# Optimization experiments

Hardware: AMD Instinct MI355X
Metric: run time of the kernel (lower is better)

The kernel has to match this reference:

```python
import jax, jax.numpy as jnp
import numpy as np

L = 4            # n_layers
D_MODEL = 768
D_STATE = 16
D_CONV = 4
EXPAND = 2
D_INNER = EXPAND * D_MODEL      # 1536
DT_RANK = (D_MODEL + 15) // 16  # 48
B = 2
T = 2048
LN_EPS = 1e-5


def setup_inputs() -> dict:
    key = jax.random.key(0)
    ks = jax.random.split(key, 12)
    s = 0.02
    x = jax.random.normal(ks[0], (B, T, D_MODEL), dtype=jnp.float32)
    in_proj_w = jax.random.normal(ks[1], (L, 2 * D_INNER, D_MODEL), dtype=jnp.float32) * s
    conv_w = jax.random.normal(ks[2], (L, D_INNER, D_CONV), dtype=jnp.float32) * s
    conv_b = jnp.zeros((L, D_INNER), dtype=jnp.float32)
    x_proj_w = jax.random.normal(ks[3], (L, DT_RANK + 2 * D_STATE, D_INNER), dtype=jnp.float32) * s
    dt_proj_w = jax.random.normal(ks[4], (L, D_INNER, DT_RANK), dtype=jnp.float32) * s
    dt_proj_b = jax.random.normal(ks[5], (L, D_INNER), dtype=jnp.float32) * 0.1
    # Standard S4D-real init: A = -[1..d_state], stored as log
    A_log = jnp.log(jnp.broadcast_to(
        jnp.arange(1, D_STATE + 1, dtype=jnp.float32), (L, D_INNER, D_STATE)))
    D_param = jnp.ones((L, D_INNER), dtype=jnp.float32)
    out_proj_w = jax.random.normal(ks[6], (L, D_MODEL, D_INNER), dtype=jnp.float32) * s
    ln_g = jnp.ones((L, D_MODEL), dtype=jnp.float32)
    ln_b = jnp.zeros((L, D_MODEL), dtype=jnp.float32)
    return {"x": x, "in_proj_w": in_proj_w, "conv_w": conv_w, "conv_b": conv_b,
            "x_proj_w": x_proj_w, "dt_proj_w": dt_proj_w, "dt_proj_b": dt_proj_b,
            "A_log": A_log, "D_param": D_param, "out_proj_w": out_proj_w,
            "ln_g": ln_g, "ln_b": ln_b}


def _layernorm(x, g, b):
    mu = jnp.mean(x, axis=-1, keepdims=True)
    var = jnp.mean(jnp.square(x - mu), axis=-1, keepdims=True)
    return (x - mu) * jax.lax.rsqrt(var + LN_EPS) * g + b


def _mamba_layer(x, inw, convw, convb, xpw, dtw, dtb, A_log, Dp, outw):
    # x: [B,T,d_model]
    Tn = x.shape[1]
    xz = jnp.einsum('btd,ed->bte', x, inw)          # [B,T,2*d_inner]
    xin, z = jnp.split(xz, 2, axis=-1)              # each [B,T,d_inner]
    # causal depthwise conv1d over time (kernel d_conv)
    xp = jnp.pad(xin, ((0, 0), (D_CONV - 1, 0), (0, 0)))
    xc = convb
    for k in range(D_CONV):
        xc = xc + xp[:, k:k + Tn, :] * convw[:, k]
    xc = jax.nn.silu(xc)                            # [B,T,d_inner]
    dbl = jnp.einsum('bti,ei->bte', xc, xpw)        # [B,T,dt_rank+2*d_state]
    dt, Bs, Cs = jnp.split(dbl, [DT_RANK, DT_RANK + D_STATE], axis=-1)
    dt = jax.nn.softplus(jnp.einsum('btr,dr->btd', dt, dtw) + dtb)  # [B,T,d_inner]
    A = -jnp.exp(A_log)                             # [d_inner,d_state]
    dA = jnp.exp(jnp.einsum('btd,dn->btdn', dt, A))  # discretized A
    dBu = (dt * xc)[..., None] * Bs[:, :, None, :]   # [B,T,d_inner,d_state]

    def step(h, inp):
        dA_t, dBu_t, C_t = inp                      # [B,d,n],[B,d,n],[B,n]
        h = dA_t * h + dBu_t
        y = jnp.einsum('bdn,bn->bd', h, C_t)
        return h, y

    h0 = jnp.zeros((x.shape[0], D_INNER, D_STATE), x.dtype)
    _, ys = jax.lax.scan(step, h0,
                         (jnp.swapaxes(dA, 0, 1), jnp.swapaxes(dBu, 0, 1),
                          jnp.swapaxes(Cs, 0, 1)))
    y = jnp.swapaxes(ys, 0, 1) + xc * Dp            # skip connection D*u
    y = y * jax.nn.silu(z)                          # gate
    return jnp.einsum('bti,ei->bte', y, outw)       # [B,T,d_model]


def reference(x, in_proj_w, conv_w, conv_b, x_proj_w, dt_proj_w, dt_proj_b,
              A_log, D_param, out_proj_w, ln_g, ln_b):
    for l in range(L):
        residual = x
        h = _mamba_layer(x, in_proj_w[l], conv_w[l], conv_b[l], x_proj_w[l],
                         dt_proj_w[l], dt_proj_b[l], A_log[l], D_param[l],
                         out_proj_w[l])
        h = _layernorm(h, ln_g[l], ln_b[l])
        x = h + residual                            # dropout=0 -> identity
    return x
```

## Files before the change

### kernel.cpp

```cpp
#include <hip/hip_runtime.h>

#define T_LEN 2048
#define DM    768
#define DI    1536
#define DS    16
#define BB    2
#define NROWS (BB * T_LEN)
#define NCH   64
#define CLEN  32

#define OFF_DTB 0
#define OFF_A   6144
#define OFF_DP  104448
#define OFF_CW  110592
#define OFF_CB  135168
#define OFF_LG  141312
#define OFF_LB  144384
#define PRM_TOT 147456

typedef __attribute__((ext_vector_type(8))) short bh8;
typedef __attribute__((ext_vector_type(4))) float f32x4;

__device__ __forceinline__ float bf2f(unsigned short u) {
    return __uint_as_float(((unsigned)u) << 16);
}
__device__ __forceinline__ unsigned short f2bf(float f) {
    unsigned u = __float_as_uint(f);
    u += 0x7FFFu + ((u >> 16) & 1u);
    return (unsigned short)(u >> 16);
}
__device__ __forceinline__ float ldin(const void* p, long i, int bf) {
    return bf ? bf2f(((const unsigned short*)p)[i]) : ((const float*)p)[i];
}

__global__ void k_sniff(const unsigned short* __restrict__ x, int* __restrict__ flag) {
    __shared__ int cnt[4];
    int tid = threadIdx.x;
    int local = 0;
#pragma unroll
    for (int j = 0; j < 4; ++j) {
        unsigned short u = x[tid * 4 + j];
        int e = (u >> 7) & 0xFF;
        if (e >= 100 && e <= 140) local++;
    }
    for (int off = 32; off; off >>= 1) local += __shfl_down(local, off, 64);
    if ((tid & 63) == 0) cnt[tid >> 6] = local;
    __syncthreads();
    if (tid == 0) {
        int tot = cnt[0] + cnt[1] + cnt[2] + cnt[3];
        *flag = (tot >= 900) ? 1 : 0;
    }
}

__global__ void k_conv_bf16(unsigned short* __restrict__ dst, const void* __restrict__ src,
                            long n, const int* __restrict__ flag) {
    int bf = *flag;
    long i = (long)blockIdx.x * 256 + threadIdx.x;
    if (i < n) dst[i] = bf ? ((const unsigned short*)src)[i] : f2bf(((const float*)src)[i]);
}

__global__ void k_convx(unsigned short* __restrict__ xbf, float* __restrict__ xf,
                        const void* __restrict__ src, const int* __restrict__ flag) {
    int bf = *flag;
    long i = (long)blockIdx.x * 256 + threadIdx.x;
    if (i < (long)NROWS * DM) {
        float v = ldin(src, i, bf);
        xbf[i] = f2bf(v);
        xf[i]  = v;
    }
}

__global__ void k_conv_xpw(unsigned short* __restrict__ dst, const void* __restrict__ src,
                           const int* __restrict__ flag) {
    int bf = *flag;
    long i = (long)blockIdx.x * 256 + threadIdx.x;
    const long total = 4L * 128 * 1536;
    if (i < total) {
        int c = (int)(i % 1536);
        long rl = i / 1536;
        int r = (int)(rl % 128);
        int l = (int)(rl / 128);
        unsigned short v = 0;
        if (r < 80) {
            long si = ((long)l * 80 + r) * 1536 + c;
            v = bf ? ((const unsigned short*)src)[si] : f2bf(((const float*)src)[si]);
        }
        dst[i] = v;
    }
}

__global__ void k_conv_dtw(unsigned short* __restrict__ dst, const void* __restrict__ src,
                           const int* __restrict__ flag) {
    int bf = *flag;
    long i = (long)blockIdx.x * 256 + threadIdx.x;
    const long total = 4L * 1536 * 64;
    if (i < total) {
        int c = (int)(i % 64);
        long rl = i / 64;
        int d = (int)(rl % 1536);
        int l = (int)(rl / 1536);
        unsigned short v = 0;
        if (c < 48) {
            long si = ((long)l * 1536 + d) * 48 + c;
            v = bf ? ((const unsigned short*)src)[si] : f2bf(((const float*)src)[si]);
        }
        dst[i] = v;
    }
}

__global__ void k_params(float* __restrict__ prm, const void* dtb, const void* alog,
                         const void* dpar, const void* cw, const void* cb,
                         const void* lg, const void* lb, const int* __restrict__ flag) {
    int bf = *flag;
    int i = blockIdx.x * 256 + threadIdx.x;
    if (i >= PRM_TOT) return;
    float v;
    if (i < OFF_A)        v = ldin(dtb, i - OFF_DTB, bf);
    else if (i < OFF_DP)  v = -__expf(ldin(alog, i - OFF_A, bf));
    else if (i < OFF_CW)  v = ldin(dpar, i - OFF_DP, bf);
    else if (i < OFF_CB)  v = ldin(cw, i - OFF_CW, bf);
    else if (i < OFF_LG)  v = ldin(cb, i - OFF_CB, bf);
    else if (i < OFF_LB)  v = ldin(lg, i - OFF_LG, bf);
    else                  v = ldin(lb, i - OFF_LB, bf);
    prm[i] = v;
}

template <int EPI>
__global__ __launch_bounds__(256) void k_gemm128(const unsigned short* __restrict__ A,
                                                 const unsigned short* __restrict__ B,
                                                 float* __restrict__ C,
                                                 int M, int N, int K) {
    __shared__ __align__(16) unsigned short As[128 * 32];
    __shared__ __align__(16) unsigned short Bs[128 * 32];
    const int tid = threadIdx.x;
    const int lane = tid & 63, wid = tid >> 6;
    const int wm = wid >> 1, wn = wid & 1;
    const long arow0 = (long)blockIdx.y * 128;
    const long bcol0 = (long)blockIdx.x * 128;
    f32x4 acc[4][4] = {};

    for (int k0 = 0; k0 < K; k0 += 32) {
#pragma unroll
        for (int j = 0; j < 2; ++j) {
            int g = (j * 256 + tid) * 8;
            int r = g >> 5, c = g & 31;
            *(int4*)&As[g] = *(const int4*)&A[(arow0 + r) * K + k0 + c];
            *(int4*)&Bs[g] = *(const int4*)&B[(bcol0 + r) * K + k0 + c];
        }
        __syncthreads();
        const int row = lane & 15, q8 = (lane >> 4) * 8;
        bh8 af[4], bfr[4];
#pragma unroll
        for (int i = 0; i < 4; ++i) af[i] = *(const bh8*)&As[(wm * 64 + i * 16 + row) * 32 + q8];
#pragma unroll
        for (int i = 0; i < 4; ++i) bfr[i] = *(const bh8*)&Bs[(wn * 64 + i * 16 + row) * 32 + q8];
#pragma unroll
        for (int i = 0; i < 4; ++i)
#pragma unroll
            for (int j = 0; j < 4; ++j)
                acc[i][j] = __builtin_amdgcn_mfma_f32_16x16x32_bf16(af[i], bfr[j], acc[i][j], 0, 0, 0);
        __syncthreads();
    }
    const int crow = (lane >> 4) * 4, ccol = lane & 15;
#pragma unroll
    for (int i = 0; i < 4; ++i)
#pragma unroll
        for (int j = 0; j < 4; ++j)
#pragma unroll
            for (int r = 0; r < 4; ++r) {
                long gr = arow0 + wm * 64 + i * 16 + crow + r;
                long gc = bcol0 + wn * 64 + j * 16 + ccol;
                C[gr * N + gc] = acc[i][j][r];
            }
}

template <int EPI>
__global__ __launch_bounds__(256) void k_gemm64(const unsigned short* __restrict__ A,
                                                const unsigned short* __restrict__ B,
                                                float* __restrict__ C,
                                                int M, int N, int K,
                                                const float* __restrict__ bias,
                                                unsigned short* __restrict__ dtlr) {
    __shared__ __align__(16) unsigned short As[64 * 32];
    __shared__ __align__(16) unsigned short Bs[64 * 32];
    const int tid = threadIdx.x;
    const int lane = tid & 63, wid = tid >> 6;
    const int wm = wid >> 1, wn = wid & 1;
    const long arow0 = (long)blockIdx.y * 64;
    const long bcol0 = (long)blockIdx.x * 64;
    f32x4 acc[2][2] = {};

    for (int k0 = 0; k0 < K; k0 += 32) {
        int g = tid * 8;
        int r = g >> 5, c = g & 31;
        *(int4*)&As[g] = *(const int4*)&A[(arow0 + r) * K + k0 + c];
        *(int4*)&Bs[g] = *(const int4*)&B[(bcol0 + r) * K + k0 + c];
        __syncthreads();
        const int row = lane & 15, q8 = (lane >> 4) * 8;
        bh8 af[2], bfr[2];
#pragma unroll
        for (int i = 0; i < 2; ++i) af[i] = *(const bh8*)&As[(wm * 32 + i * 16 + row) * 32 + q8];
#pragma unroll
        for (int i = 0; i < 2; ++i) bfr[i] = *(const bh8*)&Bs[(wn * 32 + i * 16 + row) * 32 + q8];
#pragma unroll
        for (int i = 0; i < 2; ++i)
#pragma unroll
            for (int j = 0; j < 2; ++j)
                acc[i][j] = __builtin_amdgcn_mfma_f32_16x16x32_bf16(af[i], bfr[j], acc[i][j], 0, 0, 0);
        __syncthreads();
    }
    const int crow = (lane >> 4) * 4, ccol = lane & 15;
#pragma unroll
    for (int i = 0; i < 2; ++i)
#pragma unroll
        for (int j = 0; j < 2; ++j)
#pragma unroll
            for (int r = 0; r < 4; ++r) {
                long gr = arow0 + wm * 32 + i * 16 + crow + r;
                long gc = bcol0 + wn * 32 + j * 16 + ccol;
                float v = acc[i][j][r];
                if (EPI == 1) {
                    v += bias[gc];
                    v = (v > 20.f) ? v : log1pf(__expf(v));
                }
                C[gr * N + gc] = v;
                if (EPI == 2) {
                    if (gc < 64) dtlr[gr * 64 + gc] = (gc < 48) ? f2bf(v) : (unsigned short)0;
                }
            }
}

__global__ __launch_bounds__(256) void k_conv(const float* __restrict__ xz,
                                              const float* __restrict__ cw,
                                              const float* __restrict__ cb,
                                              float* __restrict__ xc,
                                              unsigned short* __restrict__ xcbf) {
    long i = (long)blockIdx.x * 256 + threadIdx.x;
    if (i >= (long)NROWS * DI) return;
    int d = (int)(i % DI);
    long bt = i / DI;
    int t = (int)(bt & (T_LEN - 1));
    float acc = cb[d];
#pragma unroll
    for (int k = 0; k < 4; ++k) {
        int ts = t + k - 3;
        if (ts >= 0) acc += xz[(bt + k - 3) * (2 * DI) + d] * cw[d * 4 + k];
    }
    float s = acc / (1.f + __expf(-acc));
    xc[i] = s;
    xcbf[i] = f2bf(s);
}

__global__ __launch_bounds__(256) void k_scan1(const float* __restrict__ dt,
                                               const float* __restrict__ xc,
                                               const float* __restrict__ dbl,
                                               const float* __restrict__ An,
                                               float* __restrict__ hch,
                                               float* __restrict__ ppr) {
    __shared__ float BsL[CLEN * DS];
    const int tid = threadIdx.x;
    const int db = blockIdx.x % 6;
    const int c  = (blockIdx.x / 6) % NCH;
    const int b  = blockIdx.x / (6 * NCH);
    const int d  = db * 256 + tid;
    const int t0 = c * CLEN;
    for (int j = tid; j < CLEN * DS; j += 256) {
        int tt = j >> 4, nn = j & 15;
        BsL[j] = dbl[((long)b * T_LEN + t0 + tt) * 128 + 48 + nn];
    }
    __syncthreads();
    float h[DS], An_r[DS];
#pragma unroll
    for (int n = 0; n < DS; ++n) { h[n] = 0.f; An_r[n] = An[d * DS + n]; }
    float sdt = 0.f;
    for (int s = 0; s < CLEN; ++s) {
        long bt = (long)b * T_LEN + t0 + s;
        float dtv = dt[bt * DI + d];
        float xcv = xc[bt * DI + d];
        float du = dtv * xcv;
        sdt += dtv;
#pragma unroll
        for (int n = 0; n < DS; ++n) {
            float a = __expf(An_r[n] * dtv);
            h[n] = a * h[n] + du * BsL[s * DS + n];
        }
    }
    long o = (((long)b * NCH + c) * DI + d) * DS;
#pragma unroll
    for (int n = 0; n < DS; ++n) {
        hch[o + n] = h[n];
        ppr[o + n] = __expf(An_r[n] * sdt);
    }
}

__global__ __launch_bounds__(256) void k_scan2(const float* __restrict__ hch,
                                               const float* __restrict__ ppr,
                                               float* __restrict__ hin) {
    long gid = (long)blockIdx.x * 256 + threadIdx.x;
    if (gid >= (long)BB * DI * DS) return;
    int n = (int)(gid & 15);
    long r = gid >> 4;
    int d = (int)(r % DI);
    int b = (int)(r / DI);
    float h = 0.f;
    for (int c = 0; c < NCH; ++c) {
        long idx = (((long)b * NCH + c) * DI + d) * DS + n;
        hin[idx] = h;
        h = ppr[idx] * h + hch[idx];
    }
}

__global__ __launch_bounds__(256) void k_scan3(const float* __restrict__ dt,
                                               const float* __restrict__ xc,
                                               const float* __restrict__ dbl,
                                               const float* __restrict__ An,
                                               const float* __restrict__ Dp,
                                               const float* __restrict__ hin,
                                               const float* __restrict__ xz,
                                               unsigned short* __restrict__ ybf) {
    __shared__ float BsL[CLEN * DS];
    __shared__ float CsL[CLEN * DS];
    const int tid = threadIdx.x;
    const int db = blockIdx.x % 6;
    const int c  = (blockIdx.x / 6) % NCH;
    const int b  = blockIdx.x / (6 * NCH);
    const int d  = db * 256 + tid;
    const int t0 = c * CLEN;
    for (int j = tid; j < CLEN * DS; j += 256) {
        int tt = j >> 4, nn = j & 15;
        long base = ((long)b * T_LEN + t0 + tt) * 128;
        BsL[j] = dbl[base + 48 + nn];
        CsL[j] = dbl[base + 64 + nn];
    }
    __syncthreads();
    float h[DS], An_r[DS];
    long o = (((long)b * NCH + c) * DI + d) * DS;
#pragma unroll
    for (int n = 0; n < DS; ++n) { h[n] = hin[o + n]; An_r[n] = An[d * DS + n]; }
    const float dcoef = Dp[d];
    for (int s = 0; s < CLEN; ++s) {
        long bt = (long)b * T_LEN + t0 + s;
        float dtv = dt[bt * DI + d];
        float xcv = xc[bt * DI + d];
        float du = dtv * xcv;
        float y = 0.f;
#pragma unroll
        for (int n = 0; n < DS; ++n) {
            float a = __expf(An_r[n] * dtv);
            h[n] = a * h[n] + du * BsL[s * DS + n];
            y += h[n] * CsL[s * DS + n];
        }
        y += xcv * dcoef;
        float zv = xz[bt * (2 * DI) + DI + d];
        y *= zv / (1.f + __expf(-zv));
        ybf[bt * DI + d] = f2bf(y);
    }
}

__global__ __launch_bounds__(256) void k_ln(const float* __restrict__ prj,
                                            float* __restrict__ x,
                                            unsigned short* __restrict__ xbf,
                                            const float* __restrict__ lg,
                                            const float* __restrict__ lb,
                                            void* __restrict__ dout,
                                            int is_last, const int* __restrict__ flag) {
    __shared__ float red[8];
    const int row = blockIdx.x;
    const int tid = threadIdx.x;
    float v[3];
    float s = 0.f, s2 = 0.f;
#pragma unroll
    for (int j = 0; j < 3; ++j) {
        v[j] = prj[(long)row * DM + tid + j * 256];
        s += v[j];
        s2 += v[j] * v[j];
    }
    for (int off = 32; off; off >>= 1) {
        s  += __shfl_down(s, off, 64);
        s2 += __shfl_down(s2, off, 64);
    }
    if ((tid & 63) == 0) { red[tid >> 6] = s; red[4 + (tid >> 6)] = s2; }
    __syncthreads();
    float S  = red[0] + red[1] + red[2] + red[3];
    float S2 = red[4] + red[5] + red[6] + red[7];
    float mu = S * (1.f / DM);
    float var = S2 * (1.f / DM) - mu * mu;
    float rs = rsqrtf(var + 1e-5f);
    int bf = *flag;
#pragma unroll
    for (int j = 0; j < 3; ++j) {
        int e = tid + j * 256;
        long idx = (long)row * DM + e;
        float out = (v[j] - mu) * rs * lg[e] + lb[e] + x[idx];
        x[idx] = out;
        xbf[idx] = f2bf(out);
        if (is_last) {
            if (bf) ((unsigned short*)dout)[idx] = f2bf(out);
            else    ((float*)dout)[idx] = out;
        }
    }
}

extern "C" void kernel_launch(void* const* d_in, const int* in_sizes, int n_in,
                              void* d_out, int out_size, void* d_ws, size_t ws_size,
                              hipStream_t stream) {
    char* ws = (char*)d_ws;
    const size_t O_FLAG = 0;
    const size_t O_WIN  = 256;
    const size_t O_WXP  = O_WIN + 18874368;
    const size_t O_WDT  = O_WXP + 1572864;
    const size_t O_WOUT = O_WDT + 786432;
    const size_t O_PRM  = O_WOUT + 9437184;
    const size_t O_XBF  = O_PRM + 589824;
    const size_t O_XF   = O_XBF + 6291456;
    const size_t O_XZ   = O_XF + 12582912;
    const size_t O_XC   = O_XZ + 50331648;
    const size_t O_XCBF = O_XC + 25165824;
    const size_t O_DBL  = O_XCBF + 12582912;
    const size_t O_DTLR = O_DBL + 2097152;
    const size_t O_DT   = O_DTLR + 524288;
    const size_t O_HCH  = O_DT + 25165824;
    const size_t O_PPR  = O_HCH + 12582912;
    const size_t O_HIN  = O_PPR + 12582912;
    const size_t O_YBF  = O_HIN + 12582912;

    int* flag = (int*)(ws + O_FLAG);
    unsigned short* Win  = (unsigned short*)(ws + O_WIN);
    unsigned short* Wxp  = (unsigned short*)(ws + O_WXP);
    unsigned short* Wdt  = (unsigned short*)(ws + O_WDT);
    unsigned short* Wout = (unsigned short*)(ws + O_WOUT);
    float* prm = (float*)(ws + O_PRM);
    unsigned short* Xbf = (unsigned short*)(ws + O_XBF);
    float* Xf  = (float*)(ws + O_XF);
    float* Xz  = (float*)(ws + O_XZ);
    float* Xc  = (float*)(ws + O_XC);
    unsigned short* Xcbf = (unsigned short*)(ws + O_XCBF);
    float* Dbl = (float*)(ws + O_DBL);
    unsigned short* Dtlr = (unsigned short*)(ws + O_DTLR);
    float* Dt  = (float*)(ws + O_DT);
    float* Hch = (float*)(ws + O_HCH);
    float* Ppr = (float*)(ws + O_PPR);
    float* Hin = (float*)(ws + O_HIN);
    unsigned short* Ybf = (unsigned short*)(ws + O_YBF);
    float* Prj = Xz;

    const void* in_x   = d_in[0];
    const void* in_inw = d_in[1];
    const void* in_cw  = d_in[2];
    const void* in_cb  = d_in[3];
    const void* in_xpw = d_in[4];
    const void* in_dtw = d_in[5];
    const void* in_dtb = d_in[6];
    const void* in_al  = d_in[7];
    const void* in_dp  = d_in[8];
    const void* in_ow  = d_in[9];
    const void* in_lg  = d_in[10];
    const void* in_lb  = d_in[11];

    k_sniff<<<1, 256, 0, stream>>>((const unsigned short*)in_x, flag);
    k_convx<<<12288, 256, 0, stream>>>(Xbf, Xf, in_x, flag);
    k_conv_bf16<<<36864, 256, 0, stream>>>(Win, in_inw, 9437184L, flag);
    k_conv_bf16<<<18432, 256, 0, stream>>>(Wout, in_ow, 4718592L, flag);
    k_conv_xpw<<<3072, 256, 0, stream>>>(Wxp, in_xpw, flag);
    k_conv_dtw<<<1536, 256, 0, stream>>>(Wdt, in_dtw, flag);
    k_params<<<576, 256, 0, stream>>>(prm, in_dtb, in_al, in_dp, in_cw, in_cb, in_lg, in_lb, flag);

    for (int l = 0; l < 4; ++l) {
        const unsigned short* winL  = Win  + (size_t)l * 3072 * 768;
        const unsigned short* wxpL  = Wxp  + (size_t)l * 128 * 1536;
        const unsigned short* wdtL  = Wdt  + (size_t)l * 1536 * 64;
        const unsigned short* woutL = Wout + (size_t)l * 768 * 1536;
        const float* cwL  = prm + OFF_CW  + (size_t)l * DI * 4;
        const float* cbL  = prm + OFF_CB  + (size_t)l * DI;
        const float* dtbL = prm + OFF_DTB + (size_t)l * DI;
        const float* anL  = prm + OFF_A   + (size_t)l * DI * DS;
        const float* dpL  = prm + OFF_DP  + (size_t)l * DI;
        const float* lgL  = prm + OFF_LG  + (size_t)l * DM;
        const float* lbL  = prm + OFF_LB  + (size_t)l * DM;

        k_gemm128<0><<<dim3(24, 32), 256, 0, stream>>>(Xbf, winL, Xz, NROWS, 2 * DI, DM);
        k_conv<<<24576, 256, 0, stream>>>(Xz, cwL, cbL, Xc, Xcbf);
        k_gemm64<2><<<dim3(2, 64), 256, 0, stream>>>(Xcbf, wxpL, Dbl, NROWS, 128, DI, nullptr, Dtlr);
        k_gemm64<1><<<dim3(24, 64), 256, 0, stream>>>(Dtlr, wdtL, Dt, NROWS, DI, 64, dtbL, nullptr);
        k_scan1<<<768, 256, 0, stream>>>(Dt, Xc, Dbl, anL, Hch, Ppr);
        k_scan2<<<192, 256, 0, stream>>>(Hch, Ppr, Hin);
        k_scan3<<<768, 256, 0, stream>>>(Dt, Xc, Dbl, anL, dpL, Hin, Xz, Ybf);
        k_gemm64<0><<<dim3(12, 64), 256, 0, stream>>>(Ybf, woutL, Prj, NROWS, DM, DI, nullptr, nullptr);
        k_ln<<<4096, 256, 0, stream>>>(Prj, Xf, Xbf, lgL, lbL, d_out, (l == 3) ? 1 : 0, flag);
    }
}
```

Measured before the change: 1.061 ms.

## Use direct global-to-LDS GEMM loads, drop fp32 conv buffer, restructure chunked scan

The GEMM tile loads now use global_load_lds to write straight into shared memory instead of staging through registers. The fp32 copy of the conv output is removed, so the scans read the bf16 version, and scan2 recomputes chunk decay products from a per-chunk dt sum instead of storing a full products array. It also overwrites the chunk-state buffer in place. Chunks are doubled to 128 of length 16 for more scan parallelism, and B/C are read with wave-uniform vector loads instead of through LDS. In exchange the scan now sees bf16-rounded inputs, and scan2 does more sequential steps.

```diff
diff --git a/kernel.cpp b/kernel.cpp
--- a/kernel.cpp
+++ b/kernel.cpp
@@ -6,8 +6,8 @@
 #define DS    16
 #define BB    2
 #define NROWS (BB * T_LEN)
-#define NCH   64
-#define CLEN  32
+#define NCH   128
+#define CLEN  16
 
 #define OFF_DTB 0
 #define OFF_A   6144
@@ -20,6 +20,13 @@
 
 typedef __attribute__((ext_vector_type(8))) short bh8;
 typedef __attribute__((ext_vector_type(4))) float f32x4;
+
+typedef const __attribute__((address_space(1))) void as1_void;
+typedef __attribute__((address_space(3))) void as3_void;
+
+__device__ __forceinline__ void glds16(const void* g, void* l) {
+    __builtin_amdgcn_global_load_lds((as1_void*)g, (as3_void*)l, 16, 0, 0);
+}
 
 __device__ __forceinline__ float bf2f(unsigned short u) {
     return __uint_as_float(((unsigned)u) << 16);
@@ -125,7 +132,6 @@
     prm[i] = v;
 }
 
-template <int EPI>
 __global__ __launch_bounds__(256) void k_gemm128(const unsigned short* __restrict__ A,
                                                  const unsigned short* __restrict__ B,
                                                  float* __restrict__ C,
@@ -137,15 +143,17 @@
     const int wm = wid >> 1, wn = wid & 1;
     const long arow0 = (long)blockIdx.y * 128;
     const long bcol0 = (long)blockIdx.x * 128;
+    const int r16 = lane >> 2;
+    const int c8  = (lane & 3) * 8;
     f32x4 acc[4][4] = {};
 
     for (int k0 = 0; k0 < K; k0 += 32) {
 #pragma unroll
         for (int j = 0; j < 2; ++j) {
-            int g = (j * 256 + tid) * 8;
-            int r = g >> 5, c = g & 31;
-            *(int4*)&As[g] = *(const int4*)&A[(arow0 + r) * K + k0 + c];
-            *(int4*)&Bs[g] = *(const int4*)&B[(bcol0 + r) * K + k0 + c];
+            int chunk = wid + j * 4;
+            int row = chunk * 16 + r16;
+            glds16(&A[(arow0 + row) * K + k0 + c8], &As[chunk * 512]);
+            glds16(&B[(bcol0 + row) * K + k0 + c8], &Bs[chunk * 512]);
         }
         __syncthreads();
         const int row = lane & 15, q8 = (lane >> 4) * 8;
@@ -188,20 +196,21 @@
     const int wm = wid >> 1, wn = wid & 1;
     const long arow0 = (long)blockIdx.y * 64;
     const long bcol0 = (long)blockIdx.x * 64;
+    const int r16 = lane >> 2;
+    const int c8  = (lane & 3) * 8;
     f32x4 acc[2][2] = {};
 
     for (int k0 = 0; k0 < K; k0 += 32) {
-        int g = tid * 8;
-        int r = g >> 5, c = g & 31;
-        *(int4*)&As[g] = *(const int4*)&A[(arow0 + r) * K + k0 + c];
-        *(int4*)&Bs[g] = *(const int4*)&B[(bcol0 + r) * K + k0 + c];
+        int row = wid * 16 + r16;
+        glds16(&A[(arow0 + row) * K + k0 + c8], &As[wid * 512]);
+        glds16(&B[(bcol0 + row) * K + k0 + c8], &Bs[wid * 512]);
         __syncthreads();
-        const int row = lane & 15, q8 = (lane >> 4) * 8;
+        const int row2 = lane & 15, q8 = (lane >> 4) * 8;
         bh8 af[2], bfr[2];
 #pragma unroll
-        for (int i = 0; i < 2; ++i) af[i] = *(const bh8*)&As[(wm * 32 + i * 16 + row) * 32 + q8];
-#pragma unroll
-        for (int i = 0; i < 2; ++i) bfr[i] = *(const bh8*)&Bs[(wn * 32 + i * 16 + row) * 32 + q8];
+        for (int i = 0; i < 2; ++i) af[i] = *(const bh8*)&As[(wm * 32 + i * 16 + row2) * 32 + q8];
+#pragma unroll
+        for (int i = 0; i < 2; ++i) bfr[i] = *(const bh8*)&Bs[(wn * 32 + i * 16 + row2) * 32 + q8];
 #pragma unroll
         for (int i = 0; i < 2; ++i)
 #pragma unroll
@@ -233,7 +242,6 @@
 __global__ __launch_bounds__(256) void k_conv(const float* __restrict__ xz,
                                               const float* __restrict__ cw,
                                               const float* __restrict__ cb,
-                                              float* __restrict__ xc,
                                               unsigned short* __restrict__ xcbf) {
     long i = (long)blockIdx.x * 256 + threadIdx.x;
     if (i >= (long)NROWS * DI) return;
@@ -247,110 +255,131 @@
         if (ts >= 0) acc += xz[(bt + k - 3) * (2 * DI) + d] * cw[d * 4 + k];
     }
     float s = acc / (1.f + __expf(-acc));
-    xc[i] = s;
     xcbf[i] = f2bf(s);
 }
 
 __global__ __launch_bounds__(256) void k_scan1(const float* __restrict__ dt,
-                                               const float* __restrict__ xc,
+                                               const unsigned short* __restrict__ xcbf,
                                                const float* __restrict__ dbl,
                                                const float* __restrict__ An,
                                                float* __restrict__ hch,
-                                               float* __restrict__ ppr) {
-    __shared__ float BsL[CLEN * DS];
+                                               float* __restrict__ sdtb) {
     const int tid = threadIdx.x;
     const int db = blockIdx.x % 6;
     const int c  = (blockIdx.x / 6) % NCH;
     const int b  = blockIdx.x / (6 * NCH);
     const int d  = db * 256 + tid;
     const int t0 = c * CLEN;
-    for (int j = tid; j < CLEN * DS; j += 256) {
-        int tt = j >> 4, nn = j & 15;
-        BsL[j] = dbl[((long)b * T_LEN + t0 + tt) * 128 + 48 + nn];
-    }
-    __syncthreads();
     float h[DS], An_r[DS];
-#pragma unroll
-    for (int n = 0; n < DS; ++n) { h[n] = 0.f; An_r[n] = An[d * DS + n]; }
+    const f32x4* Ap = (const f32x4*)(An + (long)d * DS);
+#pragma unroll
+    for (int q = 0; q < 4; ++q) {
+        f32x4 a4 = Ap[q];
+#pragma unroll
+        for (int j = 0; j < 4; ++j) { An_r[q * 4 + j] = a4[j]; h[q * 4 + j] = 0.f; }
+    }
     float sdt = 0.f;
+    const long rowb = (long)b * T_LEN + t0;
+#pragma unroll 4
     for (int s = 0; s < CLEN; ++s) {
-        long bt = (long)b * T_LEN + t0 + s;
+        long bt = rowb + s;
         float dtv = dt[bt * DI + d];
-        float xcv = xc[bt * DI + d];
+        float xcv = bf2f(xcbf[bt * DI + d]);
+        int bi = __builtin_amdgcn_readfirstlane((int)(bt * 128 + 48));
+        const f32x4* bp = (const f32x4*)(dbl + bi);
+        float Bv[DS];
+#pragma unroll
+        for (int q = 0; q < 4; ++q) {
+            f32x4 b4 = bp[q];
+#pragma unroll
+            for (int j = 0; j < 4; ++j) Bv[q * 4 + j] = b4[j];
+        }
         float du = dtv * xcv;
         sdt += dtv;
 #pragma unroll
-        for (int n = 0; n < DS; ++n) {
-            float a = __expf(An_r[n] * dtv);
-            h[n] = a * h[n] + du * BsL[s * DS + n];
-        }
+        for (int n = 0; n < DS; ++n)
+            h[n] = __expf(An_r[n] * dtv) * h[n] + du * Bv[n];
     }
     long o = (((long)b * NCH + c) * DI + d) * DS;
-#pragma unroll
-    for (int n = 0; n < DS; ++n) {
-        hch[o + n] = h[n];
-        ppr[o + n] = __expf(An_r[n] * sdt);
-    }
-}
-
-__global__ __launch_bounds__(256) void k_scan2(const float* __restrict__ hch,
-                                               const float* __restrict__ ppr,
-                                               float* __restrict__ hin) {
+    f32x4* hp = (f32x4*)(hch + o);
+#pragma unroll
+    for (int q = 0; q < 4; ++q) {
+        f32x4 h4;
+#pragma unroll
+        for (int j = 0; j < 4; ++j) h4[j] = h[q * 4 + j];
+        hp[q] = h4;
+    }
+    sdtb[((long)b * NCH + c) * DI + d] = sdt;
+}
+
+__global__ __launch_bounds__(256) void k_scan2(float* __restrict__ hbuf,
+                                               const float* __restrict__ sdtb,
+                                               const float* __restrict__ An) {
     long gid = (long)blockIdx.x * 256 + threadIdx.x;
     if (gid >= (long)BB * DI * DS) return;
     int n = (int)(gid & 15);
     long r = gid >> 4;
     int d = (int)(r % DI);
     int b = (int)(r / DI);
+    float an = An[(long)d * DS + n];
     float h = 0.f;
     for (int c = 0; c < NCH; ++c) {
         long idx = (((long)b * NCH + c) * DI + d) * DS + n;
-        hin[idx] = h;
-        h = ppr[idx] * h + hch[idx];
+        float p = __expf(an * sdtb[((long)b * NCH + c) * DI + d]);
+        float g = hbuf[idx];
+        hbuf[idx] = h;
+        h = p * h + g;
     }
 }
 
 __global__ __launch_bounds__(256) void k_scan3(const float* __restrict__ dt,
-                                               const float* __restrict__ xc,
+                                               const unsigned short* __restrict__ xcbf,
                                                const float* __restrict__ dbl,
                                                const float* __restrict__ An,
                                                const float* __restrict__ Dp,
                                                const float* __restrict__ hin,
                                                const float* __restrict__ xz,
                                                unsigned short* __restrict__ ybf) {
-    __shared__ float BsL[CLEN * DS];
-    __shared__ float CsL[CLEN * DS];
     const int tid = threadIdx.x;
     const int db = blockIdx.x % 6;
     const int c  = (blockIdx.x / 6) % NCH;
     const int b  = blockIdx.x / (6 * NCH);
     const int d  = db * 256 + tid;
     const int t0 = c * CLEN;
-    for (int j = tid; j < CLEN * DS; j += 256) {
-        int tt = j >> 4, nn = j & 15;
-        long base = ((long)b * T_LEN + t0 + tt) * 128;
-        BsL[j] = dbl[base + 48 + nn];
-        CsL[j] = dbl[base + 64 + nn];
-    }
-    __syncthreads();
     float h[DS], An_r[DS];
     long o = (((long)b * NCH + c) * DI + d) * DS;
-#pragma unroll
-    for (int n = 0; n < DS; ++n) { h[n] = hin[o + n]; An_r[n] = An[d * DS + n]; }
+    const f32x4* Ap = (const f32x4*)(An + (long)d * DS);
+    const f32x4* Hp = (const f32x4*)(hin + o);
+#pragma unroll
+    for (int q = 0; q < 4; ++q) {
+        f32x4 a4 = Ap[q], h4 = Hp[q];
+#pragma unroll
+        for (int j = 0; j < 4; ++j) { An_r[q * 4 + j] = a4[j]; h[q * 4 + j] = h4[j]; }
+    }
     const float dcoef = Dp[d];
+    const long rowb = (long)b * T_LEN + t0;
+#pragma unroll 4
     for (int s = 0; s < CLEN; ++s) {
-        long bt = (long)b * T_LEN + t0 + s;
+        long bt = rowb + s;
         float dtv = dt[bt * DI + d];
-        float xcv = xc[bt * DI + d];
+        float xcv = bf2f(xcbf[bt * DI + d]);
+        int bi = __builtin_amdgcn_readfirstlane((int)(bt * 128 + 48));
+        const f32x4* bp = (const f32x4*)(dbl + bi);
+        float Bv[DS], Cv[DS];
+#pragma unroll
+        for (int q = 0; q < 4; ++q) {
+            f32x4 b4 = bp[q], c4 = bp[q + 4];
+#pragma unroll
+            for (int j = 0; j < 4; ++j) { Bv[q * 4 + j] = b4[j]; Cv[q * 4 + j] = c4[j]; }
+        }
         float du = dtv * xcv;
-        float y = 0.f;
+        float yp[4] = {xcv * dcoef, 0.f, 0.f, 0.f};
 #pragma unroll
         for (int n = 0; n < DS; ++n) {
-            float a = __expf(An_r[n] * dtv);
-            h[n] = a * h[n] + du * BsL[s * DS + n];
-            y += h[n] * CsL[s * DS + n];
-        }
-        y += xcv * dcoef;
+            h[n] = __expf(An_r[n] * dtv) * h[n] + du * Bv[n];
+            yp[n & 3] += h[n] * Cv[n];
+        }
+        float y = (yp[0] + yp[1]) + (yp[2] + yp[3]);
         float zv = xz[bt * (2 * DI) + DI + d];
         y *= zv / (1.f + __expf(-zv));
         ybf[bt * DI + d] = f2bf(y);
@@ -414,15 +443,13 @@
     const size_t O_XBF  = O_PRM + 589824;
     const size_t O_XF   = O_XBF + 6291456;
     const size_t O_XZ   = O_XF + 12582912;
-    const size_t O_XC   = O_XZ + 50331648;
-    const size_t O_XCBF = O_XC + 25165824;
+    const size_t O_XCBF = O_XZ + 50331648;
     const size_t O_DBL  = O_XCBF + 12582912;
     const size_t O_DTLR = O_DBL + 2097152;
     const size_t O_DT   = O_DTLR + 524288;
     const size_t O_HCH  = O_DT + 25165824;
-    const size_t O_PPR  = O_HCH + 12582912;
-    const size_t O_HIN  = O_PPR + 12582912;
-    const size_t O_YBF  = O_HIN + 12582912;
+    const size_t O_SDT  = O_HCH + 25165824;
+    const size_t O_YBF  = O_SDT + 1572864;
 
     int* flag = (int*)(ws + O_FLAG);
     unsigned short* Win  = (unsigned short*)(ws + O_WIN);
@@ -433,29 +460,20 @@
     unsigned short* Xbf = (unsigned short*)(ws + O_XBF);
     float* Xf  = (float*)(ws + O_XF);
     float* Xz  = (float*)(ws + O_XZ);
-    float* Xc  = (float*)(ws + O_XC);
     unsigned short* Xcbf = (unsigned short*)(ws + O_XCBF);
     float* Dbl = (float*)(ws + O_DBL);
     unsigned short* Dtlr = (unsigned short*)(ws + O_DTLR);
     float* Dt  = (float*)(ws + O_DT);
     float* Hch = (float*)(ws + O_HCH);
-    float* Ppr = (float*)(ws + O_PPR);
-    float* Hin = (float*)(ws + O_HIN);
+    float* Sdt = (float*)(ws + O_SDT);
     unsigned short* Ybf = (unsigned short*)(ws + O_YBF);
     float* Prj = Xz;
 
     const void* in_x   = d_in[0];
     const void* in_inw = d_in[1];
-    const void* in_cw  = d_in[2];
-    const void* in_cb  = d_in[3];
     const void* in_xpw = d_in[4];
     const void* in_dtw = d_in[5];
-    const void* in_dtb = d_in[6];
-    const void* in_al  = d_in[7];
-    const void* in_dp  = d_in[8];
     const void* in_ow  = d_in[9];
-    const void* in_lg  = d_in[10];
-    const void* in_lb  = d_in[11];
 
     k_sniff<<<1, 256, 0, stream>>>((const unsigned short*)in_x, flag);
     k_convx<<<12288, 256, 0, stream>>>(Xbf, Xf, in_x, flag);
@@ -463,7 +481,8 @@
     k_conv_bf16<<<18432, 256, 0, stream>>>(Wout, in_ow, 4718592L, flag);
     k_conv_xpw<<<3072, 256, 0, stream>>>(Wxp, in_xpw, flag);
     k_conv_dtw<<<1536, 256, 0, stream>>>(Wdt, in_dtw, flag);
-    k_params<<<576, 256, 0, stream>>>(prm, in_dtb, in_al, in_dp, in_cw, in_cb, in_lg, in_lb, flag);
+    k_params<<<576, 256, 0, stream>>>(prm, d_in[6], d_in[7], d_in[8], d_in[2], d_in[3],
+                                      d_in[10], d_in[11], flag);
 
     for (int l = 0; l < 4; ++l) {
         const unsigned short* winL  = Win  + (size_t)l * 3072 * 768;
@@ -478,13 +497,13 @@
         const float* lgL  = prm + OFF_LG  + (size_t)l * DM;
         const float* lbL  = prm + OFF_LB  + (size_t)l * DM;
 
-        k_gemm128<0><<<dim3(24, 32), 256, 0, stream>>>(Xbf, winL, Xz, NROWS, 2 * DI, DM);
-        k_conv<<<24576, 256, 0, stream>>>(Xz, cwL, cbL, Xc, Xcbf);
+        k_gemm128<<<dim3(24, 32), 256, 0, stream>>>(Xbf, winL, Xz, NROWS, 2 * DI, DM);
+        k_conv<<<24576, 256, 0, stream>>>(Xz, cwL, cbL, Xcbf);
         k_gemm64<2><<<dim3(2, 64), 256, 0, stream>>>(Xcbf, wxpL, Dbl, NROWS, 128, DI, nullptr, Dtlr);
         k_gemm64<1><<<dim3(24, 64), 256, 0, stream>>>(Dtlr, wdtL, Dt, NROWS, DI, 64, dtbL, nullptr);
-        k_scan1<<<768, 256, 0, stream>>>(Dt, Xc, Dbl, anL, Hch, Ppr);
-        k_scan2<<<192, 256, 0, stream>>>(Hch, Ppr, Hin);
-        k_scan3<<<768, 256, 0, stream>>>(Dt, Xc, Dbl, anL, dpL, Hin, Xz, Ybf);
+        k_scan1<<<BB * NCH * 6, 256, 0, stream>>>(Dt, Xcbf, Dbl, anL, Hch, Sdt);
+        k_scan2<<<192, 256, 0, stream>>>(Hch, Sdt, anL);
+        k_scan3<<<BB * NCH * 6, 256, 0, stream>>>(Dt, Xcbf, Dbl, anL, dpL, Hch, Xz, Ybf);
         k_gemm64<0><<<dim3(12, 64), 256, 0, stream>>>(Ybf, woutL, Prj, NROWS, DM, DI, nullptr, nullptr);
         k_ln<<<4096, 256, 0, stream>>>(Prj, Xf, Xbf, lgL, lbL, d_out, (l == 3) ? 1 : 0, flag);
     }
```

Result: faster. 1.021 ms (-3.8%).
